# Kernel optimization log

Hardware: AMD Instinct MI355X
Metric: run time of the kernel (lower is better)

Reference implementation:

```python
import jax, jax.numpy as jnp
import numpy as np

T, B, D, H = 512, 64, 512, 512


def lstm_cell(x, h, c, Wih, Whh, bih, bhh):
    # PyTorch LSTMCell: gates = x @ Wih.T + h @ Whh.T + bih + bhh, order [i, f, g, o]
    gates = x @ Wih.T + h @ Whh.T + (bih + bhh)
    i, f, g, o = jnp.split(gates, 4, axis=-1)
    i = jax.nn.sigmoid(i)
    f = jax.nn.sigmoid(f)
    g = jnp.tanh(g)
    o = jax.nn.sigmoid(o)
    c_new = f * c + i * g
    h_new = o * jnp.tanh(c_new)
    return h_new, c_new


def setup_inputs() -> dict:
    key = jax.random.key(0)
    ks = jax.random.split(key, 10)
    scale = 1.0 / np.sqrt(H)
    x_data = jax.random.normal(ks[0], (T, B, D), dtype=jnp.float32)
    # realistic padding mask: sorted lengths per batch element (mask[t, b] = t < len_b)
    lengths = jax.random.randint(ks[1], (B,), T // 2, T + 1)
    x_mask = (jnp.arange(T)[:, None] < lengths[None, :]).astype(jnp.float32)
    def unif(k, shape):
        return jax.random.uniform(k, shape, jnp.float32, -scale, scale)
    params = {
        'Wih_f': unif(ks[2], (4 * H, D)), 'Whh_f': unif(ks[3], (4 * H, H)),
        'bih_f': unif(ks[4], (4 * H,)),   'bhh_f': unif(ks[5], (4 * H,)),
        'Wih_r': unif(ks[6], (4 * H, D)), 'Whh_r': unif(ks[7], (4 * H, H)),
        'bih_r': unif(ks[8], (4 * H,)),   'bhh_r': unif(ks[9], (4 * H,)),
    }
    return {'x_data': x_data, 'x_mask': x_mask, **params}


def reference(x_data, x_mask, Wih_f, Whh_f, bih_f, bhh_f, Wih_r, Whh_r, bih_r, bhh_r):
    # x_data: [T, B, D], x_mask: [T, B]
    x_rev = x_data[::-1]
    m_rev = x_mask[::-1]

    def step(carry, inp):
        hf, cf, hr, cr = carry
        xf, xr, mf, mr = inp
        hf2, cf2 = lstm_cell(xf, hf, cf, Wih_f, Whh_f, bih_f, bhh_f)
        hr2, cr2 = lstm_cell(xr, hr, cr, Wih_r, Whh_r, bih_r, bhh_r)
        mf_ = mf[:, None]
        mr_ = mr[:, None]
        hf = hf2 * mf_ + hf * (1.0 - mf_)
        cf = cf2 * mf_ + cf * (1.0 - mf_)
        hr = hr2 * mr_ + hr * (1.0 - mr_)
        cr = cr2 * mr_ + cr * (1.0 - mr_)
        return (hf, cf, hr, cr), (hf, hr)

    z = jnp.zeros((B, H), dtype=x_data.dtype)
    _, (out_f, out_r) = jax.lax.scan(step, (z, z, z, z), (x_data, x_rev, x_mask, m_rev))
    # reverse outputs of the backward direction (original inserts at front)
    return jnp.concatenate([out_f, out_r[::-1]], axis=2)  # [T, B, 2H]
```

## Files before the change

### kernel.cpp

```cpp
#include <hip/hip_runtime.h>
#include <math.h>

namespace {
constexpr int T = 512, B = 64, D = 512, H = 512;
constexpr int LDSROW = D + H + 4;
}

__global__ __launch_bounds__(256) void zero_state(float* p, int n) {
  int i = blockIdx.x * 256 + threadIdx.x;
  if (i < n) p[i] = 0.f;
}

__global__ __launch_bounds__(256) void lstm_step(
    const float* __restrict__ x, const float* __restrict__ mask,
    const float* __restrict__ WihF, const float* __restrict__ WhhF,
    const float* __restrict__ bihF, const float* __restrict__ bhhF,
    const float* __restrict__ WihR, const float* __restrict__ WhhR,
    const float* __restrict__ bihR, const float* __restrict__ bhhR,
    const float* __restrict__ hPrev, float* __restrict__ hNext,
    float* __restrict__ cSt, float* __restrict__ out, int s)
{
  const int bx = blockIdx.x;
  const int d  = bx >> 7;
  const int jb = (bx >> 2) & 31;
  const int bb = bx & 3;
  const int j0 = jb * 16, b0 = bb * 16;
  const int t  = d ? (T - 1 - s) : s;

  const float* Wih = d ? WihR : WihF;
  const float* Whh = d ? WhhR : WhhF;
  const float* bih = d ? bihR : bihF;
  const float* bhh = d ? bhhR : bhhF;
  const float* hp  = hPrev + (size_t)d * B * H;
  float* hn        = hNext + (size_t)d * B * H;
  float* cp        = cSt   + (size_t)d * B * H;

  __shared__ float xh[16][LDSROW];

  const int tid = threadIdx.x;
  for (int i = tid; i < 16 * (D / 4); i += 256) {
    int row = i >> 7;
    int k4  = i & 127;
    *(float4*)&xh[row][k4 * 4] =
        *(const float4*)(x + ((size_t)t * B + b0 + row) * D + (size_t)k4 * 4);
    *(float4*)&xh[row][D + k4 * 4] =
        *(const float4*)(hp + (size_t)(b0 + row) * H + (size_t)k4 * 4);
  }
  __syncthreads();

  const int j_sub = tid >> 4, b_sub = tid & 15;
  const int j  = j0 + j_sub;
  const int bg = b0 + b_sub;

  float a0 = bih[j]         + bhh[j];
  float a1 = bih[H + j]     + bhh[H + j];
  float a2 = bih[2 * H + j] + bhh[2 * H + j];
  float a3 = bih[3 * H + j] + bhh[3 * H + j];

  const float* wi0 = Wih + (size_t)j * D;
  const float* wi1 = Wih + (size_t)(H + j) * D;
  const float* wi2 = Wih + (size_t)(2 * H + j) * D;
  const float* wi3 = Wih + (size_t)(3 * H + j) * D;

  #pragma unroll 8
  for (int k4 = 0; k4 < D / 4; ++k4) {
    float4 xv = *(const float4*)&xh[b_sub][k4 * 4];
    float4 w0 = *(const float4*)(wi0 + (size_t)k4 * 4);
    float4 w1 = *(const float4*)(wi1 + (size_t)k4 * 4);
    float4 w2 = *(const float4*)(wi2 + (size_t)k4 * 4);
    float4 w3 = *(const float4*)(wi3 + (size_t)k4 * 4);
    a0 += xv.x * w0.x + xv.y * w0.y + xv.z * w0.z + xv.w * w0.w;
    a1 += xv.x * w1.x + xv.y * w1.y + xv.z * w1.z + xv.w * w1.w;
    a2 += xv.x * w2.x + xv.y * w2.y + xv.z * w2.z + xv.w * w2.w;
    a3 += xv.x * w3.x + xv.y * w3.y + xv.z * w3.z + xv.w * w3.w;
  }

  const float* wh0 = Whh + (size_t)j * H;
  const float* wh1 = Whh + (size_t)(H + j) * H;
  const float* wh2 = Whh + (size_t)(2 * H + j) * H;
  const float* wh3 = Whh + (size_t)(3 * H + j) * H;

  #pragma unroll 8
  for (int k4 = 0; k4 < H / 4; ++k4) {
    float4 hv = *(const float4*)&xh[b_sub][D + k4 * 4];
    float4 w0 = *(const float4*)(wh0 + (size_t)k4 * 4);
    float4 w1 = *(const float4*)(wh1 + (size_t)k4 * 4);
    float4 w2 = *(const float4*)(wh2 + (size_t)k4 * 4);
    float4 w3 = *(const float4*)(wh3 + (size_t)k4 * 4);
    a0 += hv.x * w0.x + hv.y * w0.y + hv.z * w0.z + hv.w * w0.w;
    a1 += hv.x * w1.x + hv.y * w1.y + hv.z * w1.z + hv.w * w1.w;
    a2 += hv.x * w2.x + hv.y * w2.y + hv.z * w2.z + hv.w * w2.w;
    a3 += hv.x * w3.x + hv.y * w3.y + hv.z * w3.z + hv.w * w3.w;
  }

  float ig = 1.f / (1.f + expf(-a0));
  float fg = 1.f / (1.f + expf(-a1));
  float gg = tanhf(a2);
  float og = 1.f / (1.f + expf(-a3));

  float cOld = cp[(size_t)bg * H + j];
  float hOld = xh[b_sub][D + j];

  float cNew = fg * cOld + ig * gg;
  float hNew = og * tanhf(cNew);

  float m  = mask[(size_t)t * B + bg];
  float hm = hNew * m + hOld * (1.f - m);
  float cm = cNew * m + cOld * (1.f - m);

  cp[(size_t)bg * H + j] = cm;
  hn[(size_t)bg * H + j] = hm;
  out[((size_t)t * B + bg) * (2 * H) + (size_t)d * H + j] = hm;
}

extern "C" void kernel_launch(void* const* d_in, const int* in_sizes, int n_in,
                              void* d_out, int out_size, void* d_ws, size_t ws_size,
                              hipStream_t stream) {
  const float* x    = (const float*)d_in[0];
  const float* mask = (const float*)d_in[1];
  const float* WihF = (const float*)d_in[2];
  const float* WhhF = (const float*)d_in[3];
  const float* bihF = (const float*)d_in[4];
  const float* bhhF = (const float*)d_in[5];
  const float* WihR = (const float*)d_in[6];
  const float* WhhR = (const float*)d_in[7];
  const float* bihR = (const float*)d_in[8];
  const float* bhhR = (const float*)d_in[9];
  float* out = (float*)d_out;

  float* ws   = (float*)d_ws;
  float* hbuf = ws;
  float* cbuf = ws + 2 * 2 * B * H;
  int nz = 2 * 2 * B * H + 2 * B * H;
  zero_state<<<(nz + 255) / 256, 256, 0, stream>>>(ws, nz);

  for (int s = 0; s < T; ++s) {
    const float* hp = hbuf + (size_t)(s & 1) * 2 * B * H;
    float*       hn = hbuf + (size_t)((s & 1) ^ 1) * 2 * B * H;
    lstm_step<<<256, 256, 0, stream>>>(x, mask, WihF, WhhF, bihF, bhhF,
                                       WihR, WhhR, bihR, bhhR,
                                       hp, hn, cbuf, out, s);
  }
}
```

Baseline: 25.92 ms.

## Convert per-step launches into persistent cooperative kernel with LDS-resident weights

Replaces the 512 per-timestep kernel launches with one cooperative persistent kernel that uses grid.sync between timesteps. Each block keeps its 16 gate rows of Wih and Whh in LDS for the whole sequence, so weights are no longer re-read from global memory every step. Cell and hidden state for each block's slice are held in registers. x and h are streamed through double-buffered LDS chunks, and the K dimension is split across thread groups with a partial-sum reduction through LDS. In exchange it relies on all 256 blocks being co-resident and adds grid-wide barrier cost on every step.

```diff
diff --git a/kernel.cpp b/kernel.cpp
--- a/kernel.cpp
+++ b/kernel.cpp
@@ -1,116 +1,162 @@
 #include <hip/hip_runtime.h>
+#include <hip/hip_cooperative_groups.h>
 #include <math.h>
+
+namespace cg = cooperative_groups;
 
 namespace {
 constexpr int T = 512, B = 64, D = 512, H = 512;
-constexpr int LDSROW = D + H + 4;
+constexpr int WROW = 1028;
+constexpr int CHK  = 128;
+constexpr int XROW = 132;
+constexpr int WLDS = 16 * WROW;
+constexpr int XLDS = 2 * B * XROW;
+constexpr int PROW = 36;
 }
 
-__global__ __launch_bounds__(256) void zero_state(float* p, int n) {
-  int i = blockIdx.x * 256 + threadIdx.x;
-  if (i < n) p[i] = 0.f;
-}
-
-__global__ __launch_bounds__(256) void lstm_step(
+__global__ __launch_bounds__(512, 2) void bilstm_persistent(
     const float* __restrict__ x, const float* __restrict__ mask,
     const float* __restrict__ WihF, const float* __restrict__ WhhF,
     const float* __restrict__ bihF, const float* __restrict__ bhhF,
     const float* __restrict__ WihR, const float* __restrict__ WhhR,
     const float* __restrict__ bihR, const float* __restrict__ bhhR,
-    const float* __restrict__ hPrev, float* __restrict__ hNext,
-    float* __restrict__ cSt, float* __restrict__ out, int s)
+    float* __restrict__ hbuf, float* __restrict__ out)
 {
-  const int bx = blockIdx.x;
-  const int d  = bx >> 7;
-  const int jb = (bx >> 2) & 31;
-  const int bb = bx & 3;
-  const int j0 = jb * 16, b0 = bb * 16;
-  const int t  = d ? (T - 1 - s) : s;
-
-  const float* Wih = d ? WihR : WihF;
-  const float* Whh = d ? WhhR : WhhF;
-  const float* bih = d ? bihR : bihF;
-  const float* bhh = d ? bhhR : bhhF;
-  const float* hp  = hPrev + (size_t)d * B * H;
-  float* hn        = hNext + (size_t)d * B * H;
-  float* cp        = cSt   + (size_t)d * B * H;
-
-  __shared__ float xh[16][LDSROW];
+  cg::grid_group grid = cg::this_grid();
+  __shared__ float smem[WLDS + XLDS];
+  float* const wlds = smem;
+  float* const xh   = smem + WLDS;
+  float* const P    = smem + WLDS;
 
   const int tid = threadIdx.x;
-  for (int i = tid; i < 16 * (D / 4); i += 256) {
-    int row = i >> 7;
-    int k4  = i & 127;
-    *(float4*)&xh[row][k4 * 4] =
-        *(const float4*)(x + ((size_t)t * B + b0 + row) * D + (size_t)k4 * 4);
-    *(float4*)&xh[row][D + k4 * 4] =
-        *(const float4*)(hp + (size_t)(b0 + row) * H + (size_t)k4 * 4);
-  }
-  __syncthreads();
+  const int dir = (int)blockIdx.x >> 7;
+  const int j0  = ((int)blockIdx.x & 127) * 4;
 
-  const int j_sub = tid >> 4, b_sub = tid & 15;
-  const int j  = j0 + j_sub;
-  const int bg = b0 + b_sub;
+  const float* __restrict__ Wih = dir ? WihR : WihF;
+  const float* __restrict__ Whh = dir ? WhhR : WhhF;
+  const float* __restrict__ bih = dir ? bihR : bihF;
+  const float* __restrict__ bhh = dir ? bhhR : bhhF;
 
-  float a0 = bih[j]         + bhh[j];
-  float a1 = bih[H + j]     + bhh[H + j];
-  float a2 = bih[2 * H + j] + bhh[2 * H + j];
-  float a3 = bih[3 * H + j] + bhh[3 * H + j];
-
-  const float* wi0 = Wih + (size_t)j * D;
-  const float* wi1 = Wih + (size_t)(H + j) * D;
-  const float* wi2 = Wih + (size_t)(2 * H + j) * D;
-  const float* wi3 = Wih + (size_t)(3 * H + j) * D;
-
-  #pragma unroll 8
-  for (int k4 = 0; k4 < D / 4; ++k4) {
-    float4 xv = *(const float4*)&xh[b_sub][k4 * 4];
-    float4 w0 = *(const float4*)(wi0 + (size_t)k4 * 4);
-    float4 w1 = *(const float4*)(wi1 + (size_t)k4 * 4);
-    float4 w2 = *(const float4*)(wi2 + (size_t)k4 * 4);
-    float4 w3 = *(const float4*)(wi3 + (size_t)k4 * 4);
-    a0 += xv.x * w0.x + xv.y * w0.y + xv.z * w0.z + xv.w * w0.w;
-    a1 += xv.x * w1.x + xv.y * w1.y + xv.z * w1.z + xv.w * w1.w;
-    a2 += xv.x * w2.x + xv.y * w2.y + xv.z * w2.z + xv.w * w2.w;
-    a3 += xv.x * w3.x + xv.y * w3.y + xv.z * w3.z + xv.w * w3.w;
+  for (int idx = tid; idx < 16 * 256; idx += 512) {
+    const int row = idx >> 8, f4 = idx & 255;
+    const int g = row >> 2, jj = row & 3;
+    const int k = f4 * 4;
+    const float* src = (k < D)
+        ? Wih + (size_t)(g * H + j0 + jj) * D + k
+        : Whh + (size_t)(g * H + j0 + jj) * H + (k - D);
+    *(float4*)&wlds[row * WROW + k] = *(const float4*)src;
   }
 
-  const float* wh0 = Whh + (size_t)j * H;
-  const float* wh1 = Whh + (size_t)(H + j) * H;
-  const float* wh2 = Whh + (size_t)(2 * H + j) * H;
-  const float* wh3 = Whh + (size_t)(3 * H + j) * H;
-
-  #pragma unroll 8
-  for (int k4 = 0; k4 < H / 4; ++k4) {
-    float4 hv = *(const float4*)&xh[b_sub][D + k4 * 4];
-    float4 w0 = *(const float4*)(wh0 + (size_t)k4 * 4);
-    float4 w1 = *(const float4*)(wh1 + (size_t)k4 * 4);
-    float4 w2 = *(const float4*)(wh2 + (size_t)k4 * 4);
-    float4 w3 = *(const float4*)(wh3 + (size_t)k4 * 4);
-    a0 += hv.x * w0.x + hv.y * w0.y + hv.z * w0.z + hv.w * w0.w;
-    a1 += hv.x * w1.x + hv.y * w1.y + hv.z * w1.z + hv.w * w1.w;
-    a2 += hv.x * w2.x + hv.y * w2.y + hv.z * w2.z + hv.w * w2.w;
-    a3 += hv.x * w3.x + hv.y * w3.y + hv.z * w3.z + hv.w * w3.w;
+  const int fb = tid & 63, fjj = tid >> 6;
+  float bs0 = 0.f, bs1 = 0.f, bs2 = 0.f, bs3 = 0.f, cReg = 0.f, hReg = 0.f;
+  if (tid < 256) {
+    bs0 = bih[0 * H + j0 + fjj] + bhh[0 * H + j0 + fjj];
+    bs1 = bih[1 * H + j0 + fjj] + bhh[1 * H + j0 + fjj];
+    bs2 = bih[2 * H + j0 + fjj] + bhh[2 * H + j0 + fjj];
+    bs3 = bih[3 * H + j0 + fjj] + bhh[3 * H + j0 + fjj];
+    hbuf[((size_t)dir * B + fb) * H + j0 + fjj] = 0.f;
   }
 
-  float ig = 1.f / (1.f + expf(-a0));
-  float fg = 1.f / (1.f + expf(-a1));
-  float gg = tanhf(a2);
-  float og = 1.f / (1.f + expf(-a3));
+  const int bq  = tid & 15;
+  const int jjc = (tid >> 4) & 3;
+  const int kq  = tid >> 6;
 
-  float cOld = cp[(size_t)bg * H + j];
-  float hOld = xh[b_sub][D + j];
+  float4 gx0, gx1, gx2, gx3;
+  const int sb = tid >> 5, sf4 = tid & 31;
 
-  float cNew = fg * cOld + ig * gg;
-  float hNew = og * tanhf(cNew);
+  auto issue_chunk = [&](int c, int s) {
+    const int t = dir ? (T - 1 - s) : s;
+    const float* src = (c < 4)
+        ? x + (size_t)t * B * D + c * CHK
+        : hbuf + ((size_t)((s & 1) * 2 + dir) * B) * H + (c * CHK - D);
+    src += (size_t)sb * 512 + sf4 * 4;
+    gx0 = *(const float4*)(src);
+    gx1 = *(const float4*)(src + 16 * 512);
+    gx2 = *(const float4*)(src + 32 * 512);
+    gx3 = *(const float4*)(src + 48 * 512);
+  };
+  auto write_chunk = [&](int c) {
+    float* dst = xh + (c & 1) * (B * XROW) + sb * XROW + sf4 * 4;
+    *(float4*)(dst)             = gx0;
+    *(float4*)(dst + 16 * XROW) = gx1;
+    *(float4*)(dst + 32 * XROW) = gx2;
+    *(float4*)(dst + 48 * XROW) = gx3;
+  };
 
-  float m  = mask[(size_t)t * B + bg];
-  float hm = hNew * m + hOld * (1.f - m);
-  float cm = cNew * m + cOld * (1.f - m);
+  issue_chunk(0, 0);
+  grid.sync();
 
-  cp[(size_t)bg * H + j] = cm;
-  hn[(size_t)bg * H + j] = hm;
-  out[((size_t)t * B + bg) * (2 * H) + (size_t)d * H + j] = hm;
+  for (int s = 0; s < T; ++s) {
+    float acc[4][4];
+    #pragma unroll
+    for (int i = 0; i < 4; ++i)
+      #pragma unroll
+      for (int g = 0; g < 4; ++g) acc[i][g] = 0.f;
+
+    #pragma unroll 2
+    for (int c = 0; c < 8; ++c) {
+      __syncthreads();
+      write_chunk(c);
+      if (c < 7) issue_chunk(c + 1, s);
+      __syncthreads();
+      const float* wb = wlds + jjc * WROW + c * CHK + kq * 16;
+      const float* xb = xh + (c & 1) * (B * XROW) + kq * 16;
+      #pragma unroll
+      for (int k4 = 0; k4 < 4; ++k4) {
+        const int ko = k4 * 4;
+        float4 w0 = *(const float4*)(wb + 0 * 4 * WROW + ko);
+        float4 w1 = *(const float4*)(wb + 1 * 4 * WROW + ko);
+        float4 w2 = *(const float4*)(wb + 2 * 4 * WROW + ko);
+        float4 w3 = *(const float4*)(wb + 3 * 4 * WROW + ko);
+        #pragma unroll
+        for (int i = 0; i < 4; ++i) {
+          float4 hv = *(const float4*)(xb + (bq + 16 * i) * XROW + ko);
+          acc[i][0] += hv.x * w0.x + hv.y * w0.y + hv.z * w0.z + hv.w * w0.w;
+          acc[i][1] += hv.x * w1.x + hv.y * w1.y + hv.z * w1.z + hv.w * w1.w;
+          acc[i][2] += hv.x * w2.x + hv.y * w2.y + hv.z * w2.z + hv.w * w2.w;
+          acc[i][3] += hv.x * w3.x + hv.y * w3.y + hv.z * w3.z + hv.w * w3.w;
+        }
+      }
+    }
+
+    __syncthreads();
+    #pragma unroll
+    for (int i = 0; i < 4; ++i)
+      #pragma unroll
+      for (int g = 0; g < 4; ++g)
+        P[((bq + 16 * i) * 4 + jjc) * PROW + g * 8 + kq] = acc[i][g];
+    __syncthreads();
+
+    if (tid < 256) {
+      const float* pr = P + (fb * 4 + fjj) * PROW;
+      float s0 = bs0, s1 = bs1, s2 = bs2, s3 = bs3;
+      #pragma unroll
+      for (int g4 = 0; g4 < 2; ++g4) {
+        float4 a0 = *(const float4*)(pr + 0 * 8 + g4 * 4);
+        float4 a1 = *(const float4*)(pr + 1 * 8 + g4 * 4);
+        float4 a2 = *(const float4*)(pr + 2 * 8 + g4 * 4);
+        float4 a3 = *(const float4*)(pr + 3 * 8 + g4 * 4);
+        s0 += a0.x + a0.y + a0.z + a0.w;
+        s1 += a1.x + a1.y + a1.z + a1.w;
+        s2 += a2.x + a2.y + a2.z + a2.w;
+        s3 += a3.x + a3.y + a3.z + a3.w;
+      }
+      const int t = dir ? (T - 1 - s) : s;
+      const float ig = 1.f / (1.f + expf(-s0));
+      const float fg = 1.f / (1.f + expf(-s1));
+      const float gg = tanhf(s2);
+      const float og = 1.f / (1.f + expf(-s3));
+      const float cNew = fg * cReg + ig * gg;
+      const float hNew = og * tanhf(cNew);
+      const float m = mask[(size_t)t * B + fb];
+      hReg = hNew * m + hReg * (1.f - m);
+      cReg = cNew * m + cReg * (1.f - m);
+      hbuf[((size_t)(((s + 1) & 1) * 2 + dir) * B + fb) * H + j0 + fjj] = hReg;
+      out[((size_t)t * B + fb) * (2 * H) + (size_t)dir * H + j0 + fjj] = hReg;
+    }
+    if (s + 1 < T) issue_chunk(0, s + 1);
+    grid.sync();
+  }
 }
 
 extern "C" void kernel_launch(void* const* d_in, const int* in_sizes, int n_in,
@@ -126,19 +172,13 @@
   const float* WhhR = (const float*)d_in[7];
   const float* bihR = (const float*)d_in[8];
   const float* bhhR = (const float*)d_in[9];
-  float* out = (float*)d_out;
+  float* hbuf = (float*)d_ws;
+  float* outp = (float*)d_out;
 
-  float* ws   = (float*)d_ws;
-  float* hbuf = ws;
-  float* cbuf = ws + 2 * 2 * B * H;
-  int nz = 2 * 2 * B * H + 2 * B * H;
-  zero_state<<<(nz + 255) / 256, 256, 0, stream>>>(ws, nz);
-
-  for (int s = 0; s < T; ++s) {
-    const float* hp = hbuf + (size_t)(s & 1) * 2 * B * H;
-    float*       hn = hbuf + (size_t)((s & 1) ^ 1) * 2 * B * H;
-    lstm_step<<<256, 256, 0, stream>>>(x, mask, WihF, WhhF, bihF, bhhF,
-                                       WihR, WhhR, bihR, bhhR,
-                                       hp, hn, cbuf, out, s);
-  }
+  void* args[] = {(void*)&x, (void*)&mask,
+                  (void*)&WihF, (void*)&WhhF, (void*)&bihF, (void*)&bhhF,
+                  (void*)&WihR, (void*)&WhhR, (void*)&bihR, (void*)&bhhR,
+                  (void*)&hbuf, (void*)&outp};
+  hipLaunchCooperativeKernel((const void*)bilstm_persistent,
+                             dim3(256), dim3(512), args, 0, stream);
 }
```

Measured after the change: 22.62 ms. 12.7% less time.
